# Kernel tuning notes

Measured on AMD Instinct MI355X. Metric: run time of the kernel, lower is better.

The kernel has to match this reference:

```python
import jax, jax.numpy as jnp
import numpy as np

ANCHOR = 12.0      # anchor (d,h,w) size used for parametrization
NMS_IOU = 0.25     # suppression threshold
TOPK = 2048        # pre-NMS candidate cap (= stop_after), fixed for jit


def setup_inputs() -> dict:
    key = jax.random.key(0)
    k1, k2 = jax.random.split(key)
    bboxes = jax.random.normal(k1, (2, 6, 64, 96, 96), dtype=jnp.float32)
    scores = jax.random.normal(k2, (2, 64, 96, 96), dtype=jnp.float32)
    return {"bboxes": bboxes, "scores": scores}


def _deparametrize(bboxes):
    # bboxes: (B, 6, D, H, W), parametrized as in Ren et al. 2017
    D, H, W = bboxes.shape[2:]
    axes = [jnp.arange(s, dtype=bboxes.dtype) + 0.5 for s in (D, H, W)]
    zyx = jnp.stack(jnp.meshgrid(*axes, indexing='ij'))        # (3, D, H, W)
    abs_zyx = bboxes[:, :3] * ANCHOR + zyx[None]               # center coords
    abs_dhw = jnp.exp(bboxes[:, 3:]) * ANCHOR                  # sizes
    return jnp.concatenate([abs_zyx, abs_dhw], axis=1)


def _pairwise_iou(b1, b2):
    # b1: (N,6), b2: (M,6) with (z,y,x,d,h,w)
    c1, s1 = b1[:, :3], b1[:, 3:]
    c2, s2 = b2[:, :3], b2[:, 3:]
    lo = jnp.maximum((c1 - s1 / 2)[:, None, :], (c2 - s2 / 2)[None, :, :])
    hi = jnp.minimum((c1 + s1 / 2)[:, None, :], (c2 + s2 / 2)[None, :, :])
    inter = jnp.clip(hi - lo, 0).prod(-1)                      # (N, M)
    union = s1.prod(-1)[:, None] + s2.prod(-1)[None, :] - inter
    return inter / union


def _nms_one(boxes_flat, scores_flat):
    # boxes_flat: (P, 6), scores_flat: (P,)
    scores_top, idx = jax.lax.top_k(scores_flat, TOPK)
    boxes_top = boxes_flat[idx]                                # (K, 6)
    ious = _pairwise_iou(boxes_top, boxes_top)                 # (K, K)
    ar = jnp.arange(TOPK)

    def body(keep, i):
        # suppress lower-scored boxes overlapping a kept box i
        suppress = (ious[i] > NMS_IOU) & (ar > i) & keep[i]
        return keep & ~suppress, None

    keep, _ = jax.lax.scan(body, jnp.ones(TOPK, dtype=bool), ar)
    out = jnp.concatenate([scores_top[:, None], boxes_top], axis=1)  # (K, 7)
    return jnp.where(keep[:, None], out, 0.0)


def reference(bboxes, scores):
    abs_boxes = _deparametrize(bboxes)                         # (B, 6, D, H, W)
    B = bboxes.shape[0]
    boxes_flat = abs_boxes.reshape(B, 6, -1).transpose(0, 2, 1)  # (B, P, 6)
    scores_flat = scores.reshape(B, -1)                          # (B, P)
    # (B, TOPK, 7): column 0 = score, columns 1:7 = (z,y,x,d,h,w); suppressed rows zeroed
    return jax.vmap(_nms_one)(boxes_flat, scores_flat)
```

## Files before the change

kernel.cpp:

```cpp
#include <hip/hip_runtime.h>
#include <math.h>

typedef unsigned int U32;
typedef unsigned long long U64;

constexpr int N_SP   = 64 * 96 * 96;
constexpr int NBATCH = 2;
constexpr int K_TOP  = 2048;
constexpr int NBINS  = 8192;
constexpr int CAP    = 8192;
constexpr float ANCHOR_F = 12.0f;
constexpr float NMS_IOU_F = 0.25f;

constexpr size_t OFF_HIST = 0;
constexpr size_t OFF_CNT  = OFF_HIST + 2 * NBINS * 4;
constexpr size_t OFF_THR  = OFF_CNT + 256;
constexpr size_t OFF_RANK = OFF_THR + 256;
constexpr size_t OFF_CAND = OFF_RANK + 2 * CAP * 4;
constexpr size_t OFF_BOX  = OFF_CAND + 2 * CAP * 8;
constexpr size_t OFF_MASK = OFF_BOX + 2 * 14 * K_TOP * 4;

__device__ __forceinline__ U32 mono_of(float f) {
  U32 u = __float_as_uint(f);
  return (u & 0x80000000u) ? ~u : (u | 0x80000000u);
}
__device__ __forceinline__ float un_mono(U32 m) {
  U32 u = (m & 0x80000000u) ? (m ^ 0x80000000u) : ~m;
  return __uint_as_float(u);
}

__global__ void __launch_bounds__(256) k_zero(U32* hist, U32* rank, U32* cnt) {
  int g = blockIdx.x * 256 + threadIdx.x;
  hist[g] = 0;
  rank[g] = 0;
  if (g < NBATCH) cnt[g] = 0;
}

__global__ void __launch_bounds__(256) k_hist(const float* __restrict__ scores,
                                              U32* __restrict__ hist) {
  int b = blockIdx.y;
  const float4* s4 = (const float4*)(scores + (size_t)b * N_SP)
                     + (size_t)blockIdx.x * 2048 + threadIdx.x;
  float4 v[8];
#pragma unroll
  for (int e = 0; e < 8; ++e) v[e] = s4[e * 256];
  __shared__ U32 lh[NBINS];
  for (int k = threadIdx.x; k < NBINS; k += 256) lh[k] = 0;
  __syncthreads();
#pragma unroll
  for (int e = 0; e < 8; ++e) {
    atomicAdd(&lh[mono_of(v[e].x) >> 19], 1u);
    atomicAdd(&lh[mono_of(v[e].y) >> 19], 1u);
    atomicAdd(&lh[mono_of(v[e].z) >> 19], 1u);
    atomicAdd(&lh[mono_of(v[e].w) >> 19], 1u);
  }
  __syncthreads();
  U32* gh = hist + (size_t)b * NBINS;
  for (int k = threadIdx.x; k < NBINS; k += 256) {
    U32 c = lh[k];
    if (c) atomicAdd(&gh[k], c);
  }
}

__global__ void __launch_bounds__(256) k_thresh(const U32* __restrict__ hist,
                                                U32* __restrict__ thr) {
  int b = blockIdx.x;
  const U32* h = hist + (size_t)b * NBINS;
  __shared__ U32 part[256];
  int t = threadIdx.x;
  int base = NBINS - 32 * (t + 1);
  U32 s = 0;
  for (int k = 0; k < 32; ++k) s += h[base + k];
  part[t] = s;
  __syncthreads();
  if (t == 0) {
    U32 cum = 0, bin = 0;
    for (int c = 0; c < 256; ++c) {
      U32 p = part[c];
      if (cum + p >= (U32)K_TOP) {
        int hb = NBINS - 32 * c - 1;
        for (int k = 0; k < 32; ++k) {
          cum += h[hb - k];
          if (cum >= (U32)K_TOP) { bin = (U32)(hb - k); break; }
        }
        break;
      }
      cum += p;
    }
    thr[b] = bin;
  }
}

__global__ void __launch_bounds__(256) k_collect(const float* __restrict__ scores,
                                                 const U32* __restrict__ thr,
                                                 U32* __restrict__ cnt,
                                                 U64* __restrict__ cand) {
  int b = blockIdx.y;
  U32 tb = thr[b];
  const float4* s4 = (const float4*)(scores + (size_t)b * N_SP)
                     + (size_t)blockIdx.x * 1024 + threadIdx.x;
  float4 v[4];
#pragma unroll
  for (int e = 0; e < 4; ++e) v[e] = s4[e * 256];
  __shared__ U64 lbuf[4096];
  __shared__ U32 lcnt, lbase;
  if (threadIdx.x == 0) lcnt = 0;
  __syncthreads();
#pragma unroll
  for (int e = 0; e < 4; ++e) {
    U32 i0 = (blockIdx.x * 1024 + e * 256 + threadIdx.x) * 4;
    float vv[4] = {v[e].x, v[e].y, v[e].z, v[e].w};
#pragma unroll
    for (int c = 0; c < 4; ++c) {
      U32 m = mono_of(vv[c]);
      if ((m >> 19) >= tb) {
        U32 p = atomicAdd(&lcnt, 1u);
        lbuf[p] = ((U64)m << 32) | (U32)(~(i0 + c));
      }
    }
  }
  __syncthreads();
  if (threadIdx.x == 0 && lcnt) lbase = atomicAdd(&cnt[b], lcnt);
  __syncthreads();
  U32 n = lcnt;
  if (n == 0) return;
  U32 base = lbase;
  U64* cb = cand + (size_t)b * CAP;
  for (U32 k = threadIdx.x; k < n; k += 256) {
    U32 pos = base + k;
    if (pos < (U32)CAP) cb[pos] = lbuf[k];
  }
}

__global__ void __launch_bounds__(256) k_count(const U64* __restrict__ cand,
                                               const U32* __restrict__ cnt,
                                               U32* __restrict__ rank) {
  int b = blockIdx.y;
  U32 C = cnt[b]; if (C > (U32)CAP) C = CAP;
  U32 g = blockIdx.x * 256 + threadIdx.x;
  U32 t = g & (CAP - 1);
  U32 sgm = g >> 13;
  if (t >= C) return;
  const U64* cb = cand + (size_t)b * CAP;
  U64 key = cb[t];
  U32 segLen = (C + 7) >> 3;
  U32 j0 = sgm * segLen;
  U32 j1 = j0 + segLen; if (j1 > C) j1 = C;
  U32 c = 0;
  for (U32 j = j0; j < j1; ++j) c += (cb[j] > key) ? 1u : 0u;
  if (c) atomicAdd(&rank[(size_t)b * CAP + t], c);
}

#pragma clang fp contract(off)

__global__ void __launch_bounds__(256) k_gather(const float* __restrict__ bboxes,
                                                const U64* __restrict__ cand,
                                                const U32* __restrict__ cnt,
                                                const U32* __restrict__ rank,
                                                float* __restrict__ box) {
  int b = blockIdx.y;
  U32 C = cnt[b]; if (C > (U32)CAP) C = CAP;
  U32 t = blockIdx.x * 256 + threadIdx.x;
  if (t >= C) return;
  U32 r = rank[(size_t)b * CAP + t];
  if (r >= (U32)K_TOP) return;
  U64 key = cand[(size_t)b * CAP + t];
  U32 idx = ~(U32)(key & 0xFFFFFFFFull);
  float sc = un_mono((U32)(key >> 32));
  int d = idx / 9216;
  int rem = idx - d * 9216;
  int h = rem / 96;
  int w = rem - h * 96;
  const float* src = bboxes + (size_t)b * 6 * N_SP + idx;
  float r0 = src[0];
  float r1 = src[(size_t)N_SP];
  float r2 = src[(size_t)2 * N_SP];
  float r3 = src[(size_t)3 * N_SP];
  float r4 = src[(size_t)4 * N_SP];
  float r5 = src[(size_t)5 * N_SP];
  float cz = r0 * ANCHOR_F + ((float)d + 0.5f);
  float cy = r1 * ANCHOR_F + ((float)h + 0.5f);
  float cx = r2 * ANCHOR_F + ((float)w + 0.5f);
  float sz = (float)exp((double)r3) * ANCHOR_F;
  float sy = (float)exp((double)r4) * ANCHOR_F;
  float sx = (float)exp((double)r5) * ANCHOR_F;
  float* B0 = box + (size_t)b * 14 * K_TOP;
  B0[0 * K_TOP + r] = cz;  B0[1 * K_TOP + r] = cy;  B0[2 * K_TOP + r] = cx;
  B0[3 * K_TOP + r] = sz;  B0[4 * K_TOP + r] = sy;  B0[5 * K_TOP + r] = sx;
  B0[6 * K_TOP + r] = cz - sz * 0.5f;
  B0[7 * K_TOP + r] = cy - sy * 0.5f;
  B0[8 * K_TOP + r] = cx - sx * 0.5f;
  B0[9 * K_TOP + r] = cz + sz * 0.5f;
  B0[10 * K_TOP + r] = cy + sy * 0.5f;
  B0[11 * K_TOP + r] = cx + sx * 0.5f;
  B0[12 * K_TOP + r] = (sz * sy) * sx;
  B0[13 * K_TOP + r] = sc;
}

__global__ void __launch_bounds__(256) k_mask(const float* __restrict__ box,
                                              U32* __restrict__ mask) {
  int b = blockIdx.y;
  int it = blockIdx.x >> 2;
  int jq = blockIdx.x & 3;
  const float* B0 = box + (size_t)b * 14 * K_TOP;
  __shared__ float ls[7][512];
  int j0 = jq * 512;
  for (int k = threadIdx.x; k < 7 * 512; k += 256) {
    int a = k >> 9, j = k & 511;
    ls[a][j] = B0[(size_t)(6 + a) * K_TOP + j0 + j];
  }
  __syncthreads();
  int lane = threadIdx.x & 63;
  int wv = threadIdx.x >> 6;
  int i = it * 64 + lane;
  float imin0 = B0[6 * K_TOP + i], imin1 = B0[7 * K_TOP + i], imin2 = B0[8 * K_TOP + i];
  float imax0 = B0[9 * K_TOP + i], imax1 = B0[10 * K_TOP + i], imax2 = B0[11 * K_TOP + i];
  float ivol  = B0[12 * K_TOP + i];
  U32 wbits[4];
  int jb = wv * 128;
#pragma unroll
  for (int wl = 0; wl < 4; ++wl) {
    U32 bits = 0;
    for (int bit = 0; bit < 32; ++bit) {
      int jl = jb + wl * 32 + bit;
      int j = j0 + jl;
      float lo0 = fmaxf(imin0, ls[0][jl]);
      float lo1 = fmaxf(imin1, ls[1][jl]);
      float lo2 = fmaxf(imin2, ls[2][jl]);
      float hi0 = fminf(imax0, ls[3][jl]);
      float hi1 = fminf(imax1, ls[4][jl]);
      float hi2 = fminf(imax2, ls[5][jl]);
      float d0 = fmaxf(hi0 - lo0, 0.0f);
      float d1 = fmaxf(hi1 - lo1, 0.0f);
      float d2 = fmaxf(hi2 - lo2, 0.0f);
      float inter = (d0 * d1) * d2;
      float uni = (ivol + ls[6][jl]) - inter;
      float iou = inter / uni;
      bits |= ((iou > NMS_IOU_F) && (j > i)) ? (1u << bit) : 0u;
    }
    wbits[wl] = bits;
  }
  uint4* mrow = (uint4*)(mask + ((size_t)(b * K_TOP + i)) * 64);
  mrow[jq * 4 + wv] = make_uint4(wbits[0], wbits[1], wbits[2], wbits[3]);
}

__global__ void __launch_bounds__(256) k_nms(const float* __restrict__ box,
                                             const U32* __restrict__ mask,
                                             float* __restrict__ out) {
  int b = blockIdx.x;
  int tid = threadIdx.x;
  int wv = tid >> 6, lane = tid & 63;
  const U32* mk = mask + (size_t)b * K_TOP * 64;
  __shared__ U32 sbuf[2][128 * 64];
  __shared__ U32 keepArr[64];

#define STAGE(cc, FIRST, STEP)                                                 \
  do {                                                                         \
    U32* dst = sbuf[(cc) & 1];                                                 \
    const U32* gsrc = mk + (size_t)(cc) * 8192;                                \
    for (int ins = (FIRST); ins < 32; ins += (STEP)) {                         \
      __builtin_amdgcn_global_load_lds(                                        \
          (const __attribute__((address_space(1))) U32*)(gsrc + ins * 256 +    \
                                                         lane * 4),            \
          (__attribute__((address_space(3))) U32*)(dst + ins * 256), 16, 0, 0);\
    }                                                                          \
  } while (0)

  STAGE(0, wv, 4);
  __syncthreads();

  U32 keep = 0xFFFFFFFFu;
  for (int c = 0; c < 16; ++c) {
    if (wv != 0) {
      if (c + 1 < 16) STAGE(c + 1, wv - 1, 3);
    } else {
      const U32* base = sbuf[c & 1];
      for (int blk = 0; blk < 4; ++blk) {
        int g = c * 4 + blk;
        U32 rw[32];
#pragma unroll
        for (int q = 0; q < 32; ++q) rw[q] = base[(blk * 32 + q) * 64 + lane];
        U32 kw = (U32)__builtin_amdgcn_readlane((int)keep, g);
        U32 dg[32];
#pragma unroll
        for (int q = 0; q < 32; ++q)
          dg[q] = (U32)__builtin_amdgcn_readlane((int)rw[q], g);
#pragma unroll
        for (int q = 0; q < 32; ++q)
          kw = (kw & (1u << q)) ? (kw & ~dg[q]) : kw;
        U32 acc = 0;
#pragma unroll
        for (int q = 0; q < 32; ++q) {
          U32 sel = (kw & (1u << q)) ? 0xFFFFFFFFu : 0u;
          acc |= sel & rw[q];
        }
        keep &= ~acc;
      }
    }
    __syncthreads();
  }
#undef STAGE

  if (wv == 0) keepArr[lane] = keep;
  __syncthreads();

  const float* B0 = box + (size_t)b * 14 * K_TOP;
  for (int t = tid; t < K_TOP; t += 256) {
    U32 kp = (keepArr[t >> 5] >> (t & 31)) & 1u;
    float sc = B0[13 * K_TOP + t];
    float vz = B0[0 * K_TOP + t], vy = B0[1 * K_TOP + t], vx = B0[2 * K_TOP + t];
    float dz = B0[3 * K_TOP + t], dy = B0[4 * K_TOP + t], dx = B0[5 * K_TOP + t];
    float* o = out + (size_t)(b * K_TOP + t) * 7;
    o[0] = kp ? sc : 0.0f;
    o[1] = kp ? vz : 0.0f;
    o[2] = kp ? vy : 0.0f;
    o[3] = kp ? vx : 0.0f;
    o[4] = kp ? dz : 0.0f;
    o[5] = kp ? dy : 0.0f;
    o[6] = kp ? dx : 0.0f;
  }
}

extern "C" void kernel_launch(void* const* d_in, const int* in_sizes, int n_in,
                              void* d_out, int out_size, void* d_ws, size_t ws_size,
                              hipStream_t stream) {
  const float* bboxes = (const float*)d_in[0];
  const float* scores = (const float*)d_in[1];
  float* out = (float*)d_out;

  char* ws = (char*)d_ws;
  U32* hist = (U32*)(ws + OFF_HIST);
  U32* cnt  = (U32*)(ws + OFF_CNT);
  U32* thr  = (U32*)(ws + OFF_THR);
  U32* rank = (U32*)(ws + OFF_RANK);
  U64* cand = (U64*)(ws + OFF_CAND);
  float* box = (float*)(ws + OFF_BOX);
  U32* mask = (U32*)(ws + OFF_MASK);

  k_zero<<<64, 256, 0, stream>>>(hist, rank, cnt);
  k_hist<<<dim3(72, NBATCH), 256, 0, stream>>>(scores, hist);
  k_thresh<<<NBATCH, 256, 0, stream>>>(hist, thr);
  k_collect<<<dim3(144, NBATCH), 256, 0, stream>>>(scores, thr, cnt, cand);
  k_count<<<dim3(256, NBATCH), 256, 0, stream>>>(cand, cnt, rank);
  k_gather<<<dim3(CAP / 256, NBATCH), 256, 0, stream>>>(bboxes, cand, cnt, rank, box);
  k_mask<<<dim3(128, NBATCH), 256, 0, stream>>>(box, mask);
  k_nms<<<NBATCH, 256, 0, stream>>>(box, mask, out);
}
```

Baseline: 204.4 us.

## Deepen NMS mask staging to 8-slot ring with fine-grained vmcnt waits

```diff
diff --git a/kernel.cpp b/kernel.cpp
--- a/kernel.cpp
+++ b/kernel.cpp
@@ -251,14 +251,15 @@
   int tid = threadIdx.x;
   int wv = tid >> 6, lane = tid & 63;
   const U32* mk = mask + (size_t)b * K_TOP * 64;
-  __shared__ U32 sbuf[2][128 * 64];
+  __shared__ U32 sbuf[8][64 * 64];
   __shared__ U32 keepArr[64];
 
-#define STAGE(cc, FIRST, STEP)                                                 \
+#define STAGE(cc)                                                              \
   do {                                                                         \
-    U32* dst = sbuf[(cc) & 1];                                                 \
-    const U32* gsrc = mk + (size_t)(cc) * 8192;                                \
-    for (int ins = (FIRST); ins < 32; ins += (STEP)) {                         \
+    U32* dst = sbuf[(cc) & 7];                                                 \
+    const U32* gsrc = mk + (size_t)(cc) * 4096;                                \
+    _Pragma("unroll") for (int k = 0; k < 8; ++k) {                            \
+      int ins = (wv - 1) * 8 + k;                                              \
       __builtin_amdgcn_global_load_lds(                                        \
           (const __attribute__((address_space(1))) U32*)(gsrc + ins * 256 +    \
                                                          lane * 4),            \
@@ -266,17 +267,19 @@
     }                                                                          \
   } while (0)
 
-  STAGE(0, wv, 4);
-  __syncthreads();
+  if (wv == 1 || wv == 2) {
+    for (int cc = 0; cc < 6; ++cc) STAGE(cc);
+    asm volatile("s_waitcnt vmcnt(40)" ::: "memory");
+  }
+  __builtin_amdgcn_s_barrier();
+  asm volatile("" ::: "memory");
 
   U32 keep = 0xFFFFFFFFu;
-  for (int c = 0; c < 16; ++c) {
-    if (wv != 0) {
-      if (c + 1 < 16) STAGE(c + 1, wv - 1, 3);
-    } else {
-      const U32* base = sbuf[c & 1];
-      for (int blk = 0; blk < 4; ++blk) {
-        int g = c * 4 + blk;
+  for (int c = 0; c < 32; ++c) {
+    if (wv == 0) {
+      const U32* base = sbuf[c & 7];
+      for (int blk = 0; blk < 2; ++blk) {
+        int g = c * 2 + blk;
         U32 rw[32];
 #pragma unroll
         for (int q = 0; q < 32; ++q) rw[q] = base[(blk * 32 + q) * 64 + lane];
@@ -296,8 +299,19 @@
         }
         keep &= ~acc;
       }
+    } else if (wv <= 2) {
+      if (c + 6 < 32) {
+        STAGE(c + 6);
+        asm volatile("s_waitcnt vmcnt(40)" ::: "memory");
+      } else if (c == 26) { asm volatile("s_waitcnt vmcnt(32)" ::: "memory");
+      } else if (c == 27) { asm volatile("s_waitcnt vmcnt(24)" ::: "memory");
+      } else if (c == 28) { asm volatile("s_waitcnt vmcnt(16)" ::: "memory");
+      } else if (c == 29) { asm volatile("s_waitcnt vmcnt(8)"  ::: "memory");
+      } else              { asm volatile("s_waitcnt vmcnt(0)"  ::: "memory");
+      }
     }
-    __syncthreads();
+    __builtin_amdgcn_s_barrier();
+    asm volatile("" ::: "memory");
   }
 #undef STAGE
 
```

Result: faster. 198.3 us (-3.0%).

## Use sparse per-group bucket lists of nonzero mask words in NMS scan

Applied to the files above, without the earlier changes.

```diff
diff --git a/kernel.cpp b/kernel.cpp
--- a/kernel.cpp
+++ b/kernel.cpp
@@ -9,6 +9,7 @@
 constexpr int K_TOP  = 2048;
 constexpr int NBINS  = 8192;
 constexpr int CAP    = 8192;
+constexpr int CAPB   = 128;
 constexpr float ANCHOR_F = 12.0f;
 constexpr float NMS_IOU_F = 0.25f;
 
@@ -19,6 +20,9 @@
 constexpr size_t OFF_CAND = OFF_RANK + 2 * CAP * 4;
 constexpr size_t OFF_BOX  = OFF_CAND + 2 * CAP * 8;
 constexpr size_t OFF_MASK = OFF_BOX + 2 * 14 * K_TOP * 4;
+constexpr size_t OFF_DIAG = OFF_MASK + 2 * K_TOP * 64 * 4;
+constexpr size_t OFF_BCNT = OFF_DIAG + 2 * K_TOP * 4;
+constexpr size_t OFF_BKT  = OFF_BCNT + 512;
 
 __device__ __forceinline__ U32 mono_of(float f) {
   U32 u = __float_as_uint(f);
@@ -29,11 +33,13 @@
   return __uint_as_float(u);
 }
 
-__global__ void __launch_bounds__(256) k_zero(U32* hist, U32* rank, U32* cnt) {
+__global__ void __launch_bounds__(256) k_zero(U32* hist, U32* rank, U32* cnt,
+                                              U32* bcnt) {
   int g = blockIdx.x * 256 + threadIdx.x;
   hist[g] = 0;
   rank[g] = 0;
   if (g < NBATCH) cnt[g] = 0;
+  if (g < 2 * 64) bcnt[g] = 0;
 }
 
 __global__ void __launch_bounds__(256) k_hist(const float* __restrict__ scores,
@@ -198,7 +204,10 @@
 }
 
 __global__ void __launch_bounds__(256) k_mask(const float* __restrict__ box,
-                                              U32* __restrict__ mask) {
+                                              U32* __restrict__ mask,
+                                              U32* __restrict__ diag,
+                                              U32* __restrict__ bcnt,
+                                              U64* __restrict__ bkt) {
   int b = blockIdx.y;
   int it = blockIdx.x >> 2;
   int jq = blockIdx.x & 3;
@@ -242,66 +251,110 @@
   }
   uint4* mrow = (uint4*)(mask + ((size_t)(b * K_TOP + i)) * 64);
   mrow[jq * 4 + wv] = make_uint4(wbits[0], wbits[1], wbits[2], wbits[3]);
+  U32* dgp = diag + (size_t)b * K_TOP;
+  int g_src = i >> 5;
+  U32* bc = bcnt + b * 64 + g_src;
+  U64* bb = bkt + ((size_t)(b * 64 + g_src)) * CAPB;
+#pragma unroll
+  for (int wl = 0; wl < 4; ++wl) {
+    int w = jq * 16 + wv * 4 + wl;
+    if (w == (i >> 5)) dgp[i] = wbits[wl];
+    if (wbits[wl]) {
+      U32 p = atomicAdd(bc, 1u);
+      if (p < (U32)CAPB)
+        bb[p] = ((U64)((U32)((i & 31) << 6) | (U32)w) << 32) | wbits[wl];
+    }
+  }
 }
 
 __global__ void __launch_bounds__(256) k_nms(const float* __restrict__ box,
                                              const U32* __restrict__ mask,
+                                             const U32* __restrict__ diag,
+                                             const U32* __restrict__ bcnt,
+                                             const U64* __restrict__ bkt,
                                              float* __restrict__ out) {
   int b = blockIdx.x;
   int tid = threadIdx.x;
   int wv = tid >> 6, lane = tid & 63;
   const U32* mk = mask + (size_t)b * K_TOP * 64;
-  __shared__ U32 sbuf[2][128 * 64];
+  const U32* dgp = diag + (size_t)b * K_TOP;
+  const U32* bcg = bcnt + b * 64;
+  const U64* bkg = bkt + (size_t)b * 64 * CAPB;
+
+  __shared__ U32 ldiag[K_TOP];
+  __shared__ U64 lbkt[64 * CAPB];
+  __shared__ U32 lcnt[64];
   __shared__ U32 keepArr[64];
 
-#define STAGE(cc, FIRST, STEP)                                                 \
-  do {                                                                         \
-    U32* dst = sbuf[(cc) & 1];                                                 \
-    const U32* gsrc = mk + (size_t)(cc) * 8192;                                \
-    for (int ins = (FIRST); ins < 32; ins += (STEP)) {                         \
-      __builtin_amdgcn_global_load_lds(                                        \
-          (const __attribute__((address_space(1))) U32*)(gsrc + ins * 256 +    \
-                                                         lane * 4),            \
-          (__attribute__((address_space(3))) U32*)(dst + ins * 256), 16, 0, 0);\
-    }                                                                          \
-  } while (0)
-
-  STAGE(0, wv, 4);
-  __syncthreads();
-
-  U32 keep = 0xFFFFFFFFu;
-  for (int c = 0; c < 16; ++c) {
-    if (wv != 0) {
-      if (c + 1 < 16) STAGE(c + 1, wv - 1, 3);
-    } else {
-      const U32* base = sbuf[c & 1];
-      for (int blk = 0; blk < 4; ++blk) {
-        int g = c * 4 + blk;
-        U32 rw[32];
-#pragma unroll
-        for (int q = 0; q < 32; ++q) rw[q] = base[(blk * 32 + q) * 64 + lane];
+  for (int k = tid; k < K_TOP; k += 256) ldiag[k] = dgp[k];
+  {
+    U32 nc[16];
+#pragma unroll
+    for (int j = 0; j < 16; ++j) nc[j] = bcg[wv * 16 + j];
+#pragma unroll
+    for (int j = 0; j < 16; ++j) {
+      int gg = wv * 16 + j;
+      if (lane == 0) lcnt[gg] = nc[j];
+      U32 nn = nc[j] > (U32)CAPB ? (U32)CAPB : nc[j];
+      for (U32 e = (U32)lane; e < nn; e += 64)
+        lbkt[gg * CAPB + e] = bkg[(size_t)gg * CAPB + e];
+    }
+  }
+  __syncthreads();
+
+  if (wv == 0) {
+    U32 keep = 0xFFFFFFFFu;
+    U32 cnt_l = lcnt[lane];
+    bool ovf = (__ballot(cnt_l > (U32)CAPB) != 0ull);
+    if (!ovf) {
+      for (int g = 0; g < 64; ++g) {
         U32 kw = (U32)__builtin_amdgcn_readlane((int)keep, g);
-        U32 dg[32];
-#pragma unroll
-        for (int q = 0; q < 32; ++q)
-          dg[q] = (U32)__builtin_amdgcn_readlane((int)rw[q], g);
-#pragma unroll
-        for (int q = 0; q < 32; ++q)
-          kw = (kw & (1u << q)) ? (kw & ~dg[q]) : kw;
+        if (!kw) continue;
+        U32 dgl = ldiag[g * 32 + (lane & 31)];
+        U32 nzw = (U32)__ballot(dgl != 0);
+        U32 m = kw & nzw;
+        while (m) {
+          int q = __builtin_ctz(m);
+          if ((kw >> q) & 1u)
+            kw &= ~(U32)__builtin_amdgcn_readlane((int)dgl, q);
+          m &= m - 1;
+        }
+        U32 n = (U32)__builtin_amdgcn_readlane((int)cnt_l, g);
         U32 acc = 0;
-#pragma unroll
-        for (int q = 0; q < 32; ++q) {
-          U32 sel = (kw & (1u << q)) ? 0xFFFFFFFFu : 0u;
-          acc |= sel & rw[q];
+        for (U32 e0 = 0; e0 < n; e0 += 64) {
+          U64 ev = lbkt[(U32)g * CAPB + e0 + (U32)lane];
+          U32 evLo = (U32)ev, evHi = (U32)(ev >> 32);
+          U32 lim = (n - e0 > 64u) ? 64u : (n - e0);
+          for (U32 t = 0; t < lim; ++t) {
+            U32 hi = (U32)__builtin_amdgcn_readlane((int)evHi, (int)t);
+            U32 bt = (U32)__builtin_amdgcn_readlane((int)evLo, (int)t);
+            U32 il = (hi >> 6) & 31u, w = hi & 63u;
+            if ((kw >> il) & 1u)
+              acc |= (w == (U32)lane) ? bt : 0u;
+          }
         }
         keep &= ~acc;
       }
-    }
-    __syncthreads();
-  }
-#undef STAGE
-
-  if (wv == 0) keepArr[lane] = keep;
+    } else {
+      for (int g = 0; g < 64; ++g) {
+        U32 kw = (U32)__builtin_amdgcn_readlane((int)keep, g);
+        U32 dgl = ldiag[g * 32 + (lane & 31)];
+#pragma unroll
+        for (int q = 0; q < 32; ++q)
+          if ((kw >> q) & 1u)
+            kw &= ~(U32)__builtin_amdgcn_readlane((int)dgl, q);
+        U32 rw[32];
+#pragma unroll
+        for (int q = 0; q < 32; ++q)
+          rw[q] = mk[(size_t)(g * 32 + q) * 64 + lane];
+        U32 acc = 0;
+#pragma unroll
+        for (int q = 0; q < 32; ++q) acc |= ((kw >> q) & 1u) ? rw[q] : 0u;
+        keep &= ~acc;
+      }
+    }
+    keepArr[lane] = keep;
+  }
   __syncthreads();
 
   const float* B0 = box + (size_t)b * 14 * K_TOP;
@@ -336,13 +389,16 @@
   U64* cand = (U64*)(ws + OFF_CAND);
   float* box = (float*)(ws + OFF_BOX);
   U32* mask = (U32*)(ws + OFF_MASK);
-
-  k_zero<<<64, 256, 0, stream>>>(hist, rank, cnt);
+  U32* diag = (U32*)(ws + OFF_DIAG);
+  U32* bcnt = (U32*)(ws + OFF_BCNT);
+  U64* bkt  = (U64*)(ws + OFF_BKT);
+
+  k_zero<<<64, 256, 0, stream>>>(hist, rank, cnt, bcnt);
   k_hist<<<dim3(72, NBATCH), 256, 0, stream>>>(scores, hist);
   k_thresh<<<NBATCH, 256, 0, stream>>>(hist, thr);
   k_collect<<<dim3(144, NBATCH), 256, 0, stream>>>(scores, thr, cnt, cand);
   k_count<<<dim3(256, NBATCH), 256, 0, stream>>>(cand, cnt, rank);
   k_gather<<<dim3(CAP / 256, NBATCH), 256, 0, stream>>>(bboxes, cand, cnt, rank, box);
-  k_mask<<<dim3(128, NBATCH), 256, 0, stream>>>(box, mask);
-  k_nms<<<NBATCH, 256, 0, stream>>>(box, mask, out);
-}
+  k_mask<<<dim3(128, NBATCH), 256, 0, stream>>>(box, mask, diag, bcnt, bkt);
+  k_nms<<<NBATCH, 256, 0, stream>>>(box, mask, diag, bcnt, bkt, out);
+}
```

Result: faster. 182.2 us (-10.9%).
